# Kernel tuning notes

Hardware: AMD Instinct MI355X
Metric: run time of the kernel (lower is better)

Reference implementation:

```python
import jax, jax.numpy as jnp
import numpy as np

DIM = 512
HEADS = 8
HEAD_DIM = DIM // HEADS
EPS = 1e-6
LN_EPS = 1e-5


def setup_inputs() -> dict:
    key = jax.random.key(0)
    ks = jax.random.split(key, 7)
    B, S = 2, 2048
    std = 1.0 / np.sqrt(DIM)
    return {
        "x": jax.random.normal(ks[0], (B, S, DIM), dtype=jnp.float32),
        "Wq": jax.random.normal(ks[1], (DIM, DIM), dtype=jnp.float32) * std,
        "Wk": jax.random.normal(ks[2], (DIM, DIM), dtype=jnp.float32) * std,
        "Wv": jax.random.normal(ks[3], (DIM, DIM), dtype=jnp.float32) * std,
        "Wo": jax.random.normal(ks[4], (DIM, DIM), dtype=jnp.float32) * std,
        "ln_gamma": jnp.ones((DIM,), dtype=jnp.float32),
        "ln_beta": jnp.zeros((DIM,), dtype=jnp.float32),
    }


def _hardsigmoid(x):
    return jnp.clip(x / 6.0 + 0.5, 0.0, 1.0)


def _softshrink(x, lambd=0.5):
    return jnp.where(x > lambd, x - lambd, jnp.where(x < -lambd, x + lambd, 0.0))


def reference(x, Wq, Wk, Wv, Wo, ln_gamma, ln_beta):
    B, S, D = x.shape
    # torch Linear: y = x @ W.T
    q = (x @ Wq.T).reshape(B, S, HEADS, HEAD_DIM).transpose(0, 2, 1, 3)
    k = (x @ Wk.T).reshape(B, S, HEADS, HEAD_DIM).transpose(0, 2, 1, 3)
    v = (x @ Wv.T).reshape(B, S, HEADS, HEAD_DIM).transpose(0, 2, 1, 3)
    scale = 1.0 / np.sqrt(HEAD_DIM)
    scores = jnp.einsum("bhqd,bhkd->bhqk", q, k) * scale  # [B,H,S,S]
    attn_soft = jax.nn.softmax(scores, axis=-1)
    gated = attn_soft * _hardsigmoid(scores)
    attn_weights = gated / (gated.sum(axis=-1, keepdims=True) + EPS)
    attn_out = jnp.einsum("bhqk,bhkd->bhqd", attn_weights, v)
    attn_out = attn_out.transpose(0, 2, 1, 3).reshape(B, S, D)
    out = attn_out @ Wo.T
    out = out / (1.0 + jnp.abs(out))  # softsign
    out = out + _softshrink(x)
    # LayerNorm over last dim
    mu = out.mean(axis=-1, keepdims=True)
    var = ((out - mu) ** 2).mean(axis=-1, keepdims=True)
    out = (out - mu) * jax.lax.rsqrt(var + LN_EPS) * ln_gamma + ln_beta
    return out
```

## Files before the change

### kernel.cpp

```cpp
#include <hip/hip_runtime.h>

#define DIMD 512
#define NB 2
#define SEQ 2048
#define NHEADS 8
#define HDIM 64
#define MROWS (NB*SEQ)

typedef short s16x8 __attribute__((ext_vector_type(8)));
typedef float f32x4 __attribute__((ext_vector_type(4)));
typedef unsigned short u16;
typedef unsigned int u32;

__device__ __forceinline__ u16 f2bf(float f) {
    union { float f; u32 u; } c; c.f = f;
    u32 u = c.u;
    return (u16)((u + 0x7FFFu + ((u >> 16) & 1u)) >> 16);
}
__device__ __forceinline__ float bf2f(u16 v) {
    union { u32 u; float f; } c; c.u = ((u32)v) << 16;
    return c.f;
}

__device__ __forceinline__ f32x4 mfma16(s16x8 a, s16x8 b, f32x4 c) {
    return __builtin_amdgcn_mfma_f32_16x16x32_bf16(a, b, c, 0, 0, 0);
}

#define GLDS16(g, l) __builtin_amdgcn_global_load_lds( \
    (const __attribute__((address_space(1))) void*)(g), \
    (__attribute__((address_space(3))) void*)(l), 16, 0, 0)

#define ESCF 0.180336880111f
#define HSC2 0.115524530f

__global__ void cvt_all(const float* __restrict__ x, const float* __restrict__ Wq,
                        const float* __restrict__ Wk, const float* __restrict__ Wv,
                        const float* __restrict__ Wo,
                        u16* __restrict__ xb, u16* __restrict__ wqkv, u16* __restrict__ wo) {
    int i = blockIdx.x * blockDim.x + threadIdx.x;
    const float* src; u16* dst; int idx;
    if (i < 524288) { src = x; dst = xb; idx = i; }
    else {
        int jj = i - 524288;
        int which = jj >> 16; idx = jj & 65535;
        src = which == 0 ? Wq : which == 1 ? Wk : which == 2 ? Wv : Wo;
        dst = which < 3 ? wqkv + which*DIMD*DIMD : wo;
    }
    float4 v = reinterpret_cast<const float4*>(src)[idx];
    ushort4 o;
    o.x = f2bf(v.x); o.y = f2bf(v.y); o.z = f2bf(v.z); o.w = f2bf(v.w);
    reinterpret_cast<ushort4*>(dst)[idx] = o;
}

template<int WMODE>
__global__ __launch_bounds__(256) void gemm128(const u16* __restrict__ A, const u16* __restrict__ Bm,
                                               void* __restrict__ Cout, void* __restrict__ Cout2,
                                               void* __restrict__ Cout3, int M, int N, int K) {
    __shared__ u16 As[128*64];
    __shared__ u16 Bs[128*64];
    const int bm0 = blockIdx.x * 128, bn0 = blockIdx.y * 128;
    const int t = threadIdx.x;
    const int w = t >> 6, l = t & 63;
    const int lg = l >> 4, lr = l & 15;
    const int wm = w >> 1, wn = w & 1;
    f32x4 acc[4][4] = {};
    const int srow = w*32 + (l >> 3);
    const int swc = ((l & 7) ^ ((l >> 3) & 7)) * 8;
    const u16* asrc = A  + (size_t)(bm0 + srow)*K + swc;
    const u16* bsrc = Bm + (size_t)(bn0 + srow)*K + swc;
    const int ldsb = w*2048;

    for (int k0 = 0; k0 < K; k0 += 64) {
        #pragma unroll
        for (int g = 0; g < 4; g++) {
            GLDS16(asrc + (size_t)g*8*K + k0, &As[ldsb + g*512]);
            GLDS16(bsrc + (size_t)g*8*K + k0, &Bs[ldsb + g*512]);
        }
        __syncthreads();
        #pragma unroll
        for (int ks = 0; ks < 2; ks++) {
            const int swr = ((ks*4 + lg) ^ (lr & 7)) * 8;
            s16x8 af[4], bfr[4];
            #pragma unroll
            for (int fm = 0; fm < 4; fm++)
                af[fm] = *(const s16x8*)&As[(wm*64 + fm*16 + lr)*64 + swr];
            #pragma unroll
            for (int fn = 0; fn < 4; fn++)
                bfr[fn] = *(const s16x8*)&Bs[(wn*64 + fn*16 + lr)*64 + swr];
            #pragma unroll
            for (int fm = 0; fm < 4; fm++)
                #pragma unroll
                for (int fn = 0; fn < 4; fn++)
                    acc[fm][fn] = mfma16(af[fm], bfr[fn], acc[fm][fn]);
        }
        __syncthreads();
    }

    const int region = (WMODE == 3) ? (bn0 >> 9) : 0;
    const float qsc = (WMODE == 3 && region == 0) ? ESCF : 1.0f;
    #pragma unroll
    for (int fm = 0; fm < 4; fm++) {
        #pragma unroll
        for (int fn = 0; fn < 4; fn++) {
            const int mb = bm0 + wm*64 + fm*16 + lg*4;
            const int n  = bn0 + wn*64 + fn*16 + lr;
            if (WMODE == 2) {
                float* C = (float*)Cout;
                #pragma unroll
                for (int i = 0; i < 4; i++)
                    C[(size_t)(mb + i)*N + n] = acc[fm][fn][i];
            } else {
                const int nl = n & 511;
                if (region == 2) {
                    const int b = mb >> 11, s0 = mb & 2047;
                    const int h = nl >> 6, d = nl & 63;
                    ushort4 pk;
                    pk.x = f2bf(acc[fm][fn][0]);
                    pk.y = f2bf(acc[fm][fn][1]);
                    pk.z = f2bf(acc[fm][fn][2]);
                    pk.w = f2bf(acc[fm][fn][3]);
                    *(ushort4*)((u16*)Cout3 + (size_t)((b*8 + h)*64 + d)*2048 + s0) = pk;
                } else {
                    u16* C = region == 0 ? (u16*)Cout : (u16*)Cout2;
                    #pragma unroll
                    for (int i = 0; i < 4; i++)
                        C[(size_t)(mb + i)*512 + nl] = f2bf(acc[fm][fn][i] * qsc);
                }
            }
        }
    }
}

__global__ __launch_bounds__(256) void gemm_bt2(const u16* __restrict__ A, const u16* __restrict__ Bm,
                                                u16* __restrict__ Cout, int M, int N, int K) {
    __shared__ u16 As[64*64];
    __shared__ u16 Bs[64*64];
    const int bm0 = blockIdx.x * 64, bn0 = blockIdx.y * 64;
    const int t = threadIdx.x;
    const int w = t >> 6, l = t & 63;
    const int lg = l >> 4, lr = l & 15;
    const int wm = w >> 1, wn = w & 1;
    f32x4 acc[2][2] = {};
    const int srow = t >> 3;
    const int scol = (t & 7) * 8;

    for (int k0 = 0; k0 < K; k0 += 64) {
        #pragma unroll
        for (int c = 0; c < 2; c++) {
            const u16* ga = A  + (size_t)(bm0 + c*32 + srow)*K + k0 + scol;
            const u16* gb = Bm + (size_t)(bn0 + c*32 + srow)*K + k0 + scol;
            GLDS16(ga, (char*)As + c*4096 + w*1024);
            GLDS16(gb, (char*)Bs + c*4096 + w*1024);
        }
        __syncthreads();
        #pragma unroll
        for (int ks = 0; ks < 2; ks++) {
            s16x8 af[2], bfr[2];
            #pragma unroll
            for (int fm = 0; fm < 2; fm++)
                af[fm] = *(const s16x8*)&As[(wm*32 + fm*16 + lr)*64 + ks*32 + lg*8];
            #pragma unroll
            for (int fn = 0; fn < 2; fn++)
                bfr[fn] = *(const s16x8*)&Bs[(wn*32 + fn*16 + lr)*64 + ks*32 + lg*8];
            #pragma unroll
            for (int fm = 0; fm < 2; fm++)
                #pragma unroll
                for (int fn = 0; fn < 2; fn++)
                    acc[fm][fn] = mfma16(af[fm], bfr[fn], acc[fm][fn]);
        }
        __syncthreads();
    }

    #pragma unroll
    for (int fm = 0; fm < 2; fm++)
        #pragma unroll
        for (int fn = 0; fn < 2; fn++) {
            const int mb = bm0 + wm*32 + fm*16 + lg*4;
            const int n  = bn0 + wn*32 + fn*16 + lr;
            #pragma unroll
            for (int i = 0; i < 4; i++)
                Cout[(size_t)(mb + i)*N + n] = f2bf(acc[fm][fn][i]);
        }
}

__device__ __forceinline__ void attn_phase(const u16* Kc, const u16* Vc, u16* wl,
                                           s16x8 qf0, s16x8 qf1, f32x4* o, float& gacc,
                                           int kc0, int kc1, int lg, int lr) {
    f32x4 scA[4] = {};
    __builtin_amdgcn_s_setprio(1);
    #pragma unroll
    for (int n = 0; n < 4; n++) {
        s16x8 kf0 = *(const s16x8*)&Kc[(n*16 + lr)*64 + kc0];
        s16x8 kf1 = *(const s16x8*)&Kc[(n*16 + lr)*64 + kc1];
        scA[n] = mfma16(kf0, qf0, scA[n]);
        scA[n] = mfma16(kf1, qf1, scA[n]);
    }
    __builtin_amdgcn_s_setprio(0);
    #pragma unroll
    for (int n = 0; n < 4; n++) {
        #pragma unroll
        for (int i = 0; i < 4; i += 2) {
            const float s0 = scA[n][i], s1 = scA[n][i+1];
            const float e0 = exp2f(s0), e1 = exp2f(s1);
            const float h0 = __builtin_amdgcn_fmed3f(s0*HSC2 + 0.5f, 0.f, 1.f);
            const float h1 = __builtin_amdgcn_fmed3f(s1*HSC2 + 0.5f, 0.f, 1.f);
            const float w0 = e0*h0, w1 = e1*h1;
            gacc += w0 + w1;
            u32 pp;
            asm("v_cvt_pk_bf16_f32 %0, %1, %2" : "=v"(pp) : "v"(w0), "v"(w1));
            *(u32*)&wl[lr*72 + n*16 + lg*4 + i] = pp;
        }
    }
    f32x4 scB[4] = {};
    __builtin_amdgcn_s_setprio(1);
    #pragma unroll
    for (int n = 0; n < 4; n++) {
        s16x8 kf0 = *(const s16x8*)&Kc[(64 + n*16 + lr)*64 + kc0];
        s16x8 kf1 = *(const s16x8*)&Kc[(64 + n*16 + lr)*64 + kc1];
        scB[n] = mfma16(kf0, qf0, scB[n]);
        scB[n] = mfma16(kf1, qf1, scB[n]);
    }
    #pragma unroll
    for (int ks = 0; ks < 2; ks++) {
        s16x8 af = *(const s16x8*)&wl[lr*72 + ks*32 + lg*8];
        const int vcA = ((ks*4 + lg) ^ (lr & 7)) * 8;
        #pragma unroll
        for (int dn = 0; dn < 4; dn++) {
            s16x8 bvf = *(const s16x8*)&Vc[(dn*16 + lr)*128 + vcA];
            o[dn] = mfma16(af, bvf, o[dn]);
        }
    }
    __builtin_amdgcn_s_setprio(0);
    #pragma unroll
    for (int n = 0; n < 4; n++) {
        #pragma unroll
        for (int i = 0; i < 4; i += 2) {
            const float s0 = scB[n][i], s1 = scB[n][i+1];
            const float e0 = exp2f(s0), e1 = exp2f(s1);
            const float h0 = __builtin_amdgcn_fmed3f(s0*HSC2 + 0.5f, 0.f, 1.f);
            const float h1 = __builtin_amdgcn_fmed3f(s1*HSC2 + 0.5f, 0.f, 1.f);
            const float w0 = e0*h0, w1 = e1*h1;
            gacc += w0 + w1;
            u32 pp;
            asm("v_cvt_pk_bf16_f32 %0, %1, %2" : "=v"(pp) : "v"(w0), "v"(w1));
            *(u32*)&wl[lr*72 + n*16 + lg*4 + i] = pp;
        }
    }
    __builtin_amdgcn_s_setprio(1);
    #pragma unroll
    for (int ks = 0; ks < 2; ks++) {
        s16x8 af = *(const s16x8*)&wl[lr*72 + ks*32 + lg*8];
        const int vcB = ((8 + ks*4 + lg) ^ (lr & 7)) * 8;
        #pragma unroll
        for (int dn = 0; dn < 4; dn++) {
            s16x8 bvf = *(const s16x8*)&Vc[(dn*16 + lr)*128 + vcB];
            o[dn] = mfma16(af, bvf, o[dn]);
        }
    }
    __builtin_amdgcn_s_setprio(0);
}

__global__ __launch_bounds__(256) void attn_kernel(const u16* __restrict__ q, const u16* __restrict__ k,
                                                   const u16* __restrict__ vt, u16* __restrict__ attn) {
    __shared__ u16 Ks[2][128*64];
    __shared__ u16 Vs[2][64*128];
    __shared__ u16 Pl[4][16*72];
    __shared__ float invl[4][16];
    const int bid = blockIdx.x;
    const int xcd = bid & 7, j = bid >> 3;
    const int bh = 2*xcd + (j & 1);
    const int qt = j >> 1;
    const int b = bh >> 3, h = bh & 7;
    const int qb0 = qt * 64;
    const int t = threadIdx.x;
    const int w = t >> 6, l = t & 63;
    const int lg = l >> 4, lr = l & 15;

    const size_t qoff = ((size_t)(b*SEQ + qb0 + w*16 + lr))*DIMD + h*HDIM;
    s16x8 qf0 = *(const s16x8*)(q + qoff + lg*8);
    s16x8 qf1 = *(const s16x8*)(q + qoff + 32 + lg*8);

    const int kswc = ((l & 7) ^ (l >> 3)) * 8;
    const u16* ksrc = k + (size_t)b*SEQ*DIMD + h*HDIM + (size_t)(w*32 + (l >> 3))*DIMD + kswc;
    const u16* vbase = vt + (size_t)bh*HDIM*SEQ;
    int voff[4];
    #pragma unroll
    for (int g = 0; g < 4; g++) {
        const int vrow = w*16 + g*4 + (l >> 4);
        const int vc = ((l & 15) ^ (vrow & 7)) * 8;
        voff[g] = vrow*SEQ + vc;
    }
    const int ldsb = w*2048;

    f32x4 o[4] = {};
    float gacc = 0.f;
    u16* wl = &Pl[w][0];

    const int kc0 = (lg       ^ (lr & 7)) * 8;
    const int kc1 = ((4 + lg) ^ (lr & 7)) * 8;

    #pragma unroll
    for (int g = 0; g < 4; g++) {
        GLDS16(ksrc + (size_t)g*8*DIMD, &Ks[0][ldsb + g*512]);
        GLDS16(vbase + voff[g],          &Vs[0][ldsb + g*512]);
    }
    __syncthreads();

    #pragma unroll 1
    for (int tp = 0; tp < 8; ++tp) {
        const int tt0 = tp*2;
        {
            const size_t adv = (size_t)(tt0 + 1) * 128;
            #pragma unroll
            for (int g = 0; g < 4; g++) {
                GLDS16(ksrc + (adv + g*8)*DIMD, &Ks[1][ldsb + g*512]);
                GLDS16(vbase + voff[g] + adv,   &Vs[1][ldsb + g*512]);
            }
        }
        attn_phase(&Ks[0][0], &Vs[0][0], wl, qf0, qf1, o, gacc, kc0, kc1, lg, lr);
        __syncthreads();
        if (tp < 7) {
            const size_t adv = (size_t)(tt0 + 2) * 128;
            #pragma unroll
            for (int g = 0; g < 4; g++) {
                GLDS16(ksrc + (adv + g*8)*DIMD, &Ks[0][ldsb + g*512]);
                GLDS16(vbase + voff[g] + adv,   &Vs[0][ldsb + g*512]);
            }
        }
        attn_phase(&Ks[1][0], &Vs[1][0], wl, qf0, qf1, o, gacc, kc0, kc1, lg, lr);
        __syncthreads();
    }

    float tden = gacc;
    tden += __shfl_xor(tden, 16);
    tden += __shfl_xor(tden, 32);
    const float inv = 1.f / tden;
    if (l < 16) invl[w][l] = inv;
    __builtin_amdgcn_s_waitcnt(0);
    f32x4 iv = *(const f32x4*)&invl[w][lg*4];
    #pragma unroll
    for (int dn = 0; dn < 4; dn++)
        #pragma unroll
        for (int i = 0; i < 4; i++)
            attn[(size_t)(b*SEQ + qb0 + w*16 + lg*4 + i)*DIMD + h*HDIM + dn*16 + lr]
                = f2bf(o[dn][i] * iv[i]);
}

__global__ __launch_bounds__(256) void ln_epilogue(const u16* __restrict__ proj, const float* __restrict__ x,
                                                   const float* __restrict__ gamma, const float* __restrict__ beta,
                                                   float* __restrict__ out) {
    const int row = blockIdx.x*4 + (threadIdx.x >> 6);
    const int l = threadIdx.x & 63;
    const u16* pr = proj + (size_t)row*DIMD + l*8;
    const float* xr = x  + (size_t)row*DIMD + l*8;
    s16x8 pv = *(const s16x8*)pr;
    float tv[8];
    float s = 0.f, s2 = 0.f;
    #pragma unroll
    for (int j = 0; j < 2; j++) {
        float4 xv = *(const float4*)(xr + j*4);
        float xa[4] = {xv.x, xv.y, xv.z, xv.w};
        #pragma unroll
        for (int qq = 0; qq < 4; qq++) {
            const float p = bf2f((u16)pv[j*4+qq]);
            const float ss = p / (1.f + fabsf(p));
            const float xx = xa[qq];
            const float sh = xx > 0.5f ? xx - 0.5f : (xx < -0.5f ? xx + 0.5f : 0.f);
            const float tt = ss + sh;
            tv[j*4+qq] = tt; s += tt; s2 += tt*tt;
        }
    }
    #pragma unroll
    for (int m = 1; m < 64; m <<= 1) { s += __shfl_xor(s, m); s2 += __shfl_xor(s2, m); }
    const float mu = s * (1.f/512.f);
    float var = s2 * (1.f/512.f) - mu*mu;
    const float rstd = rsqrtf(var + 1e-5f);
    #pragma unroll
    for (int j = 0; j < 2; j++) {
        float4 g  = *(const float4*)(gamma + l*8 + j*4);
        float4 bb = *(const float4*)(beta  + l*8 + j*4);
        float4 ov;
        ov.x = (tv[j*4+0]-mu)*rstd*g.x + bb.x;
        ov.y = (tv[j*4+1]-mu)*rstd*g.y + bb.y;
        ov.z = (tv[j*4+2]-mu)*rstd*g.z + bb.z;
        ov.w = (tv[j*4+3]-mu)*rstd*g.w + bb.w;
        *(float4*)(out + (size_t)row*DIMD + l*8 + j*4) = ov;
    }
}

extern "C" void kernel_launch(void* const* d_in, const int* in_sizes, int n_in,
                              void* d_out, int out_size, void* d_ws, size_t ws_size,
                              hipStream_t stream) {
    const float* x     = (const float*)d_in[0];
    const float* Wq    = (const float*)d_in[1];
    const float* Wk    = (const float*)d_in[2];
    const float* Wv    = (const float*)d_in[3];
    const float* Wo    = (const float*)d_in[4];
    const float* gamma = (const float*)d_in[5];
    const float* beta  = (const float*)d_in[6];
    float* out = (float*)d_out;
    char* ws = (char*)d_ws;

    u16* xb    = (u16*)(ws);
    u16* wqkvb = (u16*)(ws + (4<<20));
    u16* wob   = (u16*)(ws + (4<<20) + (1536<<10));
    u16* qb    = (u16*)(ws + (6<<20));
    u16* kb    = (u16*)(ws + (10<<20));
    u16* vtb   = (u16*)(ws + (14<<20));
    u16* ab    = (u16*)(ws + (18<<20));
    u16* proj  = (u16*)(ws + (22<<20));

    cvt_all<<<3072, 256, 0, stream>>>(x, Wq, Wk, Wv, Wo, xb, wqkvb, wob);

    gemm128<3><<<dim3(MROWS/128, 1536/128), 256, 0, stream>>>(xb, wqkvb, qb, kb, vtb, MROWS, 1536, DIMD);

    attn_kernel<<<SEQ/64 * NB*NHEADS, 256, 0, stream>>>(qb, kb, vtb, ab);

    gemm_bt2<<<dim3(MROWS/64, DIMD/64), 256, 0, stream>>>(ab, wob, proj, MROWS, DIMD, DIMD);

    ln_epilogue<<<MROWS/4, 256, 0, stream>>>(proj, x, gamma, beta, out);
}
```

Before: 76.06 us.

## Rewrite attention with 32x32 MFMA, register P via permlane, and split-K combine

```diff
diff --git a/kernel.cpp b/kernel.cpp
--- a/kernel.cpp
+++ b/kernel.cpp
@@ -9,6 +9,7 @@
 
 typedef short s16x8 __attribute__((ext_vector_type(8)));
 typedef float f32x4 __attribute__((ext_vector_type(4)));
+typedef float f32x16 __attribute__((ext_vector_type(16)));
 typedef unsigned short u16;
 typedef unsigned int u32;
 
@@ -24,6 +25,9 @@
 
 __device__ __forceinline__ f32x4 mfma16(s16x8 a, s16x8 b, f32x4 c) {
     return __builtin_amdgcn_mfma_f32_16x16x32_bf16(a, b, c, 0, 0, 0);
+}
+__device__ __forceinline__ f32x16 mfma32(s16x8 a, s16x8 b, f32x16 c) {
+    return __builtin_amdgcn_mfma_f32_32x32x16_bf16(a, b, c, 0, 0, 0);
 }
 
 #define GLDS16(g, l) __builtin_amdgcn_global_load_lds( \
@@ -183,106 +187,79 @@
         }
 }
 
-__device__ __forceinline__ void attn_phase(const u16* Kc, const u16* Vc, u16* wl,
-                                           s16x8 qf0, s16x8 qf1, f32x4* o, float& gacc,
-                                           int kc0, int kc1, int lg, int lr) {
-    f32x4 scA[4] = {};
-    __builtin_amdgcn_s_setprio(1);
-    #pragma unroll
-    for (int n = 0; n < 4; n++) {
-        s16x8 kf0 = *(const s16x8*)&Kc[(n*16 + lr)*64 + kc0];
-        s16x8 kf1 = *(const s16x8*)&Kc[(n*16 + lr)*64 + kc1];
-        scA[n] = mfma16(kf0, qf0, scA[n]);
-        scA[n] = mfma16(kf1, qf1, scA[n]);
-    }
-    __builtin_amdgcn_s_setprio(0);
-    #pragma unroll
-    for (int n = 0; n < 4; n++) {
-        #pragma unroll
-        for (int i = 0; i < 4; i += 2) {
-            const float s0 = scA[n][i], s1 = scA[n][i+1];
-            const float e0 = exp2f(s0), e1 = exp2f(s1);
-            const float h0 = __builtin_amdgcn_fmed3f(s0*HSC2 + 0.5f, 0.f, 1.f);
-            const float h1 = __builtin_amdgcn_fmed3f(s1*HSC2 + 0.5f, 0.f, 1.f);
-            const float w0 = e0*h0, w1 = e1*h1;
-            gacc += w0 + w1;
-            u32 pp;
-            asm("v_cvt_pk_bf16_f32 %0, %1, %2" : "=v"(pp) : "v"(w0), "v"(w1));
-            *(u32*)&wl[lr*72 + n*16 + lg*4 + i] = pp;
-        }
-    }
-    f32x4 scB[4] = {};
-    __builtin_amdgcn_s_setprio(1);
-    #pragma unroll
-    for (int n = 0; n < 4; n++) {
-        s16x8 kf0 = *(const s16x8*)&Kc[(64 + n*16 + lr)*64 + kc0];
-        s16x8 kf1 = *(const s16x8*)&Kc[(64 + n*16 + lr)*64 + kc1];
-        scB[n] = mfma16(kf0, qf0, scB[n]);
-        scB[n] = mfma16(kf1, qf1, scB[n]);
-    }
-    #pragma unroll
-    for (int ks = 0; ks < 2; ks++) {
-        s16x8 af = *(const s16x8*)&wl[lr*72 + ks*32 + lg*8];
-        const int vcA = ((ks*4 + lg) ^ (lr & 7)) * 8;
-        #pragma unroll
-        for (int dn = 0; dn < 4; dn++) {
-            s16x8 bvf = *(const s16x8*)&Vc[(dn*16 + lr)*128 + vcA];
-            o[dn] = mfma16(af, bvf, o[dn]);
-        }
-    }
-    __builtin_amdgcn_s_setprio(0);
-    #pragma unroll
-    for (int n = 0; n < 4; n++) {
-        #pragma unroll
-        for (int i = 0; i < 4; i += 2) {
-            const float s0 = scB[n][i], s1 = scB[n][i+1];
-            const float e0 = exp2f(s0), e1 = exp2f(s1);
-            const float h0 = __builtin_amdgcn_fmed3f(s0*HSC2 + 0.5f, 0.f, 1.f);
-            const float h1 = __builtin_amdgcn_fmed3f(s1*HSC2 + 0.5f, 0.f, 1.f);
-            const float w0 = e0*h0, w1 = e1*h1;
-            gacc += w0 + w1;
-            u32 pp;
-            asm("v_cvt_pk_bf16_f32 %0, %1, %2" : "=v"(pp) : "v"(w0), "v"(w1));
-            *(u32*)&wl[lr*72 + n*16 + lg*4 + i] = pp;
-        }
-    }
-    __builtin_amdgcn_s_setprio(1);
-    #pragma unroll
-    for (int ks = 0; ks < 2; ks++) {
-        s16x8 af = *(const s16x8*)&wl[lr*72 + ks*32 + lg*8];
-        const int vcB = ((8 + ks*4 + lg) ^ (lr & 7)) * 8;
-        #pragma unroll
-        for (int dn = 0; dn < 4; dn++) {
-            s16x8 bvf = *(const s16x8*)&Vc[(dn*16 + lr)*128 + vcB];
-            o[dn] = mfma16(af, bvf, o[dn]);
-        }
-    }
-    __builtin_amdgcn_s_setprio(0);
-}
-
-__global__ __launch_bounds__(256) void attn_kernel(const u16* __restrict__ q, const u16* __restrict__ k,
-                                                   const u16* __restrict__ vt, u16* __restrict__ attn) {
+__device__ __forceinline__ void attn_phase32(const u16* Kc, const u16* Vc, const s16x8* qf,
+                                             f32x16& o0, f32x16& o1, float& gacc,
+                                             int ln, int hi, int l7) {
+    #pragma unroll
+    for (int kb = 0; kb < 4; kb++) {
+        f32x16 sc = {};
+        __builtin_amdgcn_s_setprio(1);
+        #pragma unroll
+        for (int c = 0; c < 4; c++) {
+            s16x8 kf = *(const s16x8*)&Kc[(kb*32 + ln)*64 + (((c << 1) | hi) ^ l7)*8];
+            sc = mfma32(kf, qf[c], sc);
+        }
+        __builtin_amdgcn_s_setprio(0);
+        u32 u[4][2];
+        #pragma unroll
+        for (int b2 = 0; b2 < 4; b2++) {
+            float ww[4];
+            #pragma unroll
+            for (int r = 0; r < 4; r++) {
+                const float s = sc[b2*4 + r];
+                const float e = exp2f(s);
+                const float hs = __builtin_amdgcn_fmed3f(s*HSC2 + 0.5f, 0.f, 1.f);
+                ww[r] = e*hs;
+            }
+            gacc += (ww[0] + ww[1]) + (ww[2] + ww[3]);
+            asm("v_cvt_pk_bf16_f32 %0, %1, %2" : "=v"(u[b2][0]) : "v"(ww[0]), "v"(ww[1]));
+            asm("v_cvt_pk_bf16_f32 %0, %1, %2" : "=v"(u[b2][1]) : "v"(ww[2]), "v"(ww[3]));
+        }
+        #pragma unroll
+        for (int c16 = 0; c16 < 2; c16++) {
+            u32 x0 = u[2*c16][0], y0 = u[2*c16+1][0];
+            u32 x1 = u[2*c16][1], y1 = u[2*c16+1][1];
+            asm("v_permlane32_swap_b32 %0, %1" : "+v"(x0), "+v"(y0));
+            asm("v_permlane32_swap_b32 %0, %1" : "+v"(x1), "+v"(y1));
+            union { u32 uu[4]; s16x8 v; } pa;
+            pa.uu[0] = x0; pa.uu[1] = x1; pa.uu[2] = y0; pa.uu[3] = y1;
+            const int ccv = kb*4 + c16*2 + hi;
+            s16x8 vf0 = *(const s16x8*)&Vc[(size_t)ln*128        + (ccv ^ l7)*8];
+            s16x8 vf1 = *(const s16x8*)&Vc[(size_t)(32 + ln)*128 + (ccv ^ l7)*8];
+            __builtin_amdgcn_s_setprio(1);
+            o0 = mfma32(pa.v, vf0, o0);
+            o1 = mfma32(pa.v, vf1, o1);
+            __builtin_amdgcn_s_setprio(0);
+        }
+    }
+}
+
+__global__ __launch_bounds__(256) void attn_split(const u16* __restrict__ q, const u16* __restrict__ k,
+                                                  const u16* __restrict__ vt,
+                                                  float* __restrict__ opart, float* __restrict__ gpart) {
     __shared__ u16 Ks[2][128*64];
     __shared__ u16 Vs[2][64*128];
-    __shared__ u16 Pl[4][16*72];
-    __shared__ float invl[4][16];
     const int bid = blockIdx.x;
     const int xcd = bid & 7, j = bid >> 3;
-    const int bh = 2*xcd + (j & 1);
-    const int qt = j >> 1;
+    const int g4 = j >> 4, qt = j & 15;
+    const int bhks = xcd*4 + g4;
+    const int bh = bhks >> 1, ks = bhks & 1;
     const int b = bh >> 3, h = bh & 7;
-    const int qb0 = qt * 64;
+    const int qb0 = qt * 128;
     const int t = threadIdx.x;
     const int w = t >> 6, l = t & 63;
-    const int lg = l >> 4, lr = l & 15;
-
-    const size_t qoff = ((size_t)(b*SEQ + qb0 + w*16 + lr))*DIMD + h*HDIM;
-    s16x8 qf0 = *(const s16x8*)(q + qoff + lg*8);
-    s16x8 qf1 = *(const s16x8*)(q + qoff + 32 + lg*8);
-
-    const int kswc = ((l & 7) ^ (l >> 3)) * 8;
-    const u16* ksrc = k + (size_t)b*SEQ*DIMD + h*HDIM + (size_t)(w*32 + (l >> 3))*DIMD + kswc;
-    const u16* vbase = vt + (size_t)bh*HDIM*SEQ;
+    const int ln = l & 31, hi = l >> 5, l7 = l & 7;
+
+    const size_t qrow = (size_t)(b*SEQ + qb0 + w*32 + ln);
+    s16x8 qf[4];
+    #pragma unroll
+    for (int c = 0; c < 4; c++)
+        qf[c] = *(const s16x8*)(q + qrow*DIMD + h*HDIM + c*16 + hi*8);
+
+    const int srow = w*32 + (l >> 3);
+    const int kswc = (l7 ^ (l >> 3)) * 8;
+    const u16* ksrc = k + (size_t)(b*SEQ + ks*1024 + srow)*DIMD + h*HDIM + kswc;
+    const u16* vbase = vt + (size_t)bh*HDIM*SEQ + ks*1024;
     int voff[4];
     #pragma unroll
     for (int g = 0; g < 4; g++) {
@@ -292,12 +269,8 @@
     }
     const int ldsb = w*2048;
 
-    f32x4 o[4] = {};
+    f32x16 o0 = {}, o1 = {};
     float gacc = 0.f;
-    u16* wl = &Pl[w][0];
-
-    const int kc0 = (lg       ^ (lr & 7)) * 8;
-    const int kc1 = ((4 + lg) ^ (lr & 7)) * 8;
 
     #pragma unroll
     for (int g = 0; g < 4; g++) {
@@ -307,7 +280,7 @@
     __syncthreads();
 
     #pragma unroll 1
-    for (int tp = 0; tp < 8; ++tp) {
+    for (int tp = 0; tp < 4; ++tp) {
         const int tt0 = tp*2;
         {
             const size_t adv = (size_t)(tt0 + 1) * 128;
@@ -317,9 +290,9 @@
                 GLDS16(vbase + voff[g] + adv,   &Vs[1][ldsb + g*512]);
             }
         }
-        attn_phase(&Ks[0][0], &Vs[0][0], wl, qf0, qf1, o, gacc, kc0, kc1, lg, lr);
-        __syncthreads();
-        if (tp < 7) {
+        attn_phase32(&Ks[0][0], &Vs[0][0], qf, o0, o1, gacc, ln, hi, l7);
+        __syncthreads();
+        if (tp < 3) {
             const size_t adv = (size_t)(tt0 + 2) * 128;
             #pragma unroll
             for (int g = 0; g < 4; g++) {
@@ -327,23 +300,41 @@
                 GLDS16(vbase + voff[g] + adv,   &Vs[0][ldsb + g*512]);
             }
         }
-        attn_phase(&Ks[1][0], &Vs[1][0], wl, qf0, qf1, o, gacc, kc0, kc1, lg, lr);
-        __syncthreads();
-    }
-
-    float tden = gacc;
-    tden += __shfl_xor(tden, 16);
-    tden += __shfl_xor(tden, 32);
-    const float inv = 1.f / tden;
-    if (l < 16) invl[w][l] = inv;
-    __builtin_amdgcn_s_waitcnt(0);
-    f32x4 iv = *(const f32x4*)&invl[w][lg*4];
-    #pragma unroll
-    for (int dn = 0; dn < 4; dn++)
-        #pragma unroll
-        for (int i = 0; i < 4; i++)
-            attn[(size_t)(b*SEQ + qb0 + w*16 + lg*4 + i)*DIMD + h*HDIM + dn*16 + lr]
-                = f2bf(o[dn][i] * iv[i]);
+        attn_phase32(&Ks[1][0], &Vs[1][0], qf, o0, o1, gacc, ln, hi, l7);
+        __syncthreads();
+    }
+
+    gacc += __shfl_xor(gacc, 32);
+    if (l < 32)
+        gpart[((size_t)ks*16 + bh)*SEQ + qb0 + w*32 + l] = gacc;
+
+    float* op = opart + ((size_t)ks*MROWS + b*SEQ + qb0 + w*32)*DIMD + h*HDIM;
+    #pragma unroll
+    for (int i = 0; i < 16; i++) {
+        const int qr = (i & 3) + 8*(i >> 2) + 4*hi;
+        op[(size_t)qr*DIMD + ln]      = o0[i];
+        op[(size_t)qr*DIMD + 32 + ln] = o1[i];
+    }
+}
+
+__global__ __launch_bounds__(256) void attn_combine(const float* __restrict__ opart,
+                                                    const float* __restrict__ gpart,
+                                                    u16* __restrict__ attn) {
+    const int idx = blockIdx.x*256 + threadIdx.x;
+    const int row = idx >> 7;
+    const int col = (idx & 127) * 4;
+    const int b = row >> 11, s = row & 2047, h = col >> 6;
+    const float g = gpart[((size_t)(b*8 + h))*SEQ + s]
+                  + gpart[((size_t)(16 + b*8 + h))*SEQ + s];
+    const float inv = 1.f / g;
+    const float4 a0 = *(const float4*)(opart + (size_t)row*DIMD + col);
+    const float4 a1 = *(const float4*)(opart + ((size_t)MROWS + row)*DIMD + col);
+    ushort4 r;
+    r.x = f2bf((a0.x + a1.x)*inv);
+    r.y = f2bf((a0.y + a1.y)*inv);
+    r.z = f2bf((a0.z + a1.z)*inv);
+    r.w = f2bf((a0.w + a1.w)*inv);
+    *(ushort4*)(attn + (size_t)row*DIMD + col) = r;
 }
 
 __global__ __launch_bounds__(256) void ln_epilogue(const u16* __restrict__ proj, const float* __restrict__ x,
@@ -409,12 +400,15 @@
     u16* vtb   = (u16*)(ws + (14<<20));
     u16* ab    = (u16*)(ws + (18<<20));
     u16* proj  = (u16*)(ws + (22<<20));
+    float* opart = (float*)(ws + (26<<20));
+    float* gpart = (float*)(ws + (42<<20));
 
     cvt_all<<<3072, 256, 0, stream>>>(x, Wq, Wk, Wv, Wo, xb, wqkvb, wob);
 
     gemm128<3><<<dim3(MROWS/128, 1536/128), 256, 0, stream>>>(xb, wqkvb, qb, kb, vtb, MROWS, 1536, DIMD);
 
-    attn_kernel<<<SEQ/64 * NB*NHEADS, 256, 0, stream>>>(qb, kb, vtb, ab);
+    attn_split<<<512, 256, 0, stream>>>(qb, kb, vtb, opart, gpart);
+    attn_combine<<<2048, 256, 0, stream>>>(opart, gpart, ab);
 
     gemm_bt2<<<dim3(MROWS/64, DIMD/64), 256, 0, stream>>>(ab, wob, proj, MROWS, DIMD, DIMD);
 
```

After: 76.95 us. No clear change (+1.2%).
